# Kernel tuning notes

Measured on AMD Instinct MI355X. Metric: run time of the kernel, lower is better.

Reference implementation:

```python
import jax, jax.numpy as jnp
import numpy as np

N, E, D_IN, D_HID, D_OUT, G = 50000, 800000, 64, 64, 64, 64
BN_EPS = 1e-5


def gcn_conv(x, W, b, src, dst, n_nodes):
    """PyG GCNConv: add self-loops, sym-normalized sum aggregation, then bias.
    out_i = sum_{j->i} d_j^-1/2 d_i^-1/2 (x W)_j + d_i^-1 (x W)_i + b
    where d_i = 1 + in-degree(i) (self-loop included)."""
    h = x @ W  # [N, out]
    deg = jax.ops.segment_sum(jnp.ones((src.shape[0],), h.dtype), dst,
                              num_segments=n_nodes) + 1.0  # self-loop
    dinv = jax.lax.rsqrt(deg)  # deg >= 1 always
    coef = dinv[src] * dinv[dst]  # [E]
    msgs = h[src] * coef[:, None]  # [E, out] -- the big gather
    agg = jax.ops.segment_sum(msgs, dst, num_segments=n_nodes)
    agg = agg + h * (dinv * dinv)[:, None]  # self-loop messages
    return agg + b


def global_mean_pool(x, batch, n_graphs):
    sums = jax.ops.segment_sum(x, batch, num_segments=n_graphs)
    cnts = jax.ops.segment_sum(jnp.ones((x.shape[0],), x.dtype), batch,
                               num_segments=n_graphs)
    return sums / jnp.maximum(cnts, 1.0)[:, None]


def setup_inputs() -> dict:
    key = jax.random.key(0)
    ks = jax.random.split(key, 8)
    x = jax.random.normal(ks[0], (N, D_IN), dtype=jnp.float32)
    edge_index = jax.random.randint(ks[1], (2, E), 0, N, dtype=jnp.int32)
    batch = jnp.sort(jax.random.randint(ks[2], (N,), 0, G, dtype=jnp.int32))
    s1 = 1.0 / np.sqrt(D_IN)
    s2 = 1.0 / np.sqrt(D_HID)
    W1 = jax.random.uniform(ks[3], (D_IN, D_HID), jnp.float32, -s1, s1)
    b1 = jnp.zeros((D_HID,), jnp.float32)
    gamma = jnp.ones((D_HID,), jnp.float32)
    beta = jnp.zeros((D_HID,), jnp.float32)
    W2 = jax.random.uniform(ks[4], (D_HID, D_OUT), jnp.float32, -s2, s2)
    b2 = jnp.zeros((D_OUT,), jnp.float32)
    return {"x": x, "edge_index": edge_index, "batch": batch,
            "W1": W1, "b1": b1, "gamma": gamma, "beta": beta,
            "W2": W2, "b2": b2}


def reference(x, edge_index, batch, W1, b1, gamma, beta, W2, b2):
    src, dst = edge_index[0], edge_index[1]
    h = gcn_conv(x, W1, b1, src, dst, N)
    # BatchNorm1d with batch statistics (training-mode forward)
    mu = jnp.mean(h, axis=0)
    var = jnp.mean(jnp.square(h - mu), axis=0)
    h = (h - mu) * jax.lax.rsqrt(var + BN_EPS) * gamma + beta
    h = jax.nn.elu(h)
    # dropout is identity in eval / deterministic reference
    out = gcn_conv(h, W2, b2, src, dst, N)
    graph_rep = global_mean_pool(out, batch, G)
    return (out, graph_rep)
```

## Files before the change

kernel.cpp:

```cpp
#include <hip/hip_runtime.h>


constexpr int GGRAPHS = 64;
constexpr int EPB = 8192;

__global__ void cnt_kernel(const int* __restrict__ batch, int* __restrict__ cnt, int n) {
  __shared__ int h[GGRAPHS];
  int t = threadIdx.x;
  if (t < GGRAPHS) h[t] = 0;
  __syncthreads();
  for (int i = blockIdx.x * 256 + t; i < n; i += gridDim.x * 256) {
    int g = batch[i];
    if ((unsigned)g < (unsigned)GGRAPHS) atomicAdd(&h[g], 1);
  }
  __syncthreads();
  if (t < GGRAPHS && h[t] > 0) atomicAdd(&cnt[t], h[t]);
}

__global__ void phist_kernel(const int* __restrict__ dst, int* __restrict__ hist,
                             int E, int n, int nblk, int nbuck) {
  __shared__ int h[256];
  int t = threadIdx.x;
  h[t] = 0;
  __syncthreads();
  int e0 = blockIdx.x * EPB;
  int e1 = e0 + EPB < E ? e0 + EPB : E;
  for (int i = e0 + t; i < e1; i += 256) {
    int d = dst[i];
    if ((unsigned)d < (unsigned)n) atomicAdd(&h[d >> 8], 1);
  }
  __syncthreads();
  if (t < nbuck) hist[t * nblk + blockIdx.x] = h[t];
}

__global__ void scan1_kernel(const int* __restrict__ in, int* __restrict__ out,
                             int* __restrict__ bsum, int n) {
  __shared__ int tmp[256];
  int t = threadIdx.x;
  int i = blockIdx.x * 256 + t;
  int v = (i < n) ? in[i] : 0;
  tmp[t] = v;
  __syncthreads();
#pragma unroll
  for (int off = 1; off < 256; off <<= 1) {
    int a = (t >= off) ? tmp[t - off] : 0;
    __syncthreads();
    tmp[t] += a;
    __syncthreads();
  }
  if (i < n) out[i] = tmp[t] - v;
  if (t == 255) bsum[blockIdx.x] = tmp[255];
}

__global__ void scan2_kernel(int* __restrict__ bsum, int nb) {
  __shared__ int tmp[256];
  int t = threadIdx.x;
  int v = (t < nb) ? bsum[t] : 0;
  tmp[t] = v;
  __syncthreads();
#pragma unroll
  for (int off = 1; off < 256; off <<= 1) {
    int a = (t >= off) ? tmp[t - off] : 0;
    __syncthreads();
    tmp[t] += a;
    __syncthreads();
  }
  if (t < nb) bsum[t] = tmp[t] - v;
  if (t == 255) bsum[nb] = tmp[255];
}

__global__ void scan_add_kernel(int* __restrict__ data, const int* __restrict__ bsum,
                                int S, int nbt) {
  int i = blockIdx.x * 256 + threadIdx.x;
  if (i < S) data[i] += bsum[blockIdx.x];
  if (i == 0) data[S] = bsum[nbt];
}

__global__ void part_kernel(const int* __restrict__ srcp, const int* __restrict__ dstp,
                            const int* __restrict__ hist, int* __restrict__ part,
                            int E, int n, int nblk, int nbuck) {
  __shared__ int cur[256];
  int t = threadIdx.x;
  if (t < nbuck) cur[t] = hist[t * nblk + blockIdx.x];
  __syncthreads();
  int e0 = blockIdx.x * EPB;
  int e1 = e0 + EPB < E ? e0 + EPB : E;
  for (int i = e0 + t; i < e1; i += 256) {
    int d = dstp[i];
    if ((unsigned)d >= (unsigned)n) continue;
    int s = srcp[i];
    int pos = atomicAdd(&cur[d >> 8], 1);
    part[pos] = (s << 8) | (d & 255);
  }
}

__global__ void csr_kernel(const int* __restrict__ part, const int* __restrict__ hist,
                           int* __restrict__ rowptr, float* __restrict__ dinv,
                           int* __restrict__ col, int n, int nblk, int nbuck) {
  __shared__ int degL[256], scn[256], cur[256];
  int t = threadIdx.x;
  int b = blockIdx.x;
  degL[t] = 0;
  cur[t] = 0;
  __syncthreads();
  int base = hist[b * nblk];
  int end = hist[(b + 1) * nblk];
  for (int i = base + t; i < end; i += 256) atomicAdd(&degL[part[i] & 255], 1);
  __syncthreads();
  int dv = degL[t];
  scn[t] = dv;
  __syncthreads();
#pragma unroll
  for (int off = 1; off < 256; off <<= 1) {
    int a = (t >= off) ? scn[t - off] : 0;
    __syncthreads();
    scn[t] += a;
    __syncthreads();
  }
  int excl = scn[t] - dv;
  int node = (b << 8) + t;
  if (node < n) {
    rowptr[node] = base + excl;
    dinv[node] = rsqrtf((float)dv + 1.0f);
  }
  if (b == nbuck - 1 && t == 0) rowptr[n] = end;
  scn[t] = excl;
  __syncthreads();
  for (int i = base + t; i < end; i += 256) {
    int u = part[i];
    int d = u & 255;
    int k = atomicAdd(&cur[d], 1);
    col[base + scn[d] + k] = u >> 8;
  }
}

__global__ void mm64_kernel(const float* __restrict__ X, const float* __restrict__ W,
                            float* __restrict__ Y, int n) {
  __shared__ float Ws[64][64];
  __shared__ float xs[4][64];
  int tid = threadIdx.x;
  for (int i = tid; i < 64 * 64; i += 256) Ws[i >> 6][i & 63] = W[i];
  int rr = tid >> 6, c = tid & 63;
  int row = blockIdx.x * 4 + rr;
  xs[rr][c] = (row < n) ? X[row * 64 + c] : 0.0f;
  __syncthreads();
  float acc = 0.0f;
#pragma unroll
  for (int k = 0; k < 64; ++k) acc = fmaf(xs[rr][k], Ws[k][c], acc);
  if (row < n) Y[row * 64 + c] = acc;
}

__global__ void bn_elu_mm64_kernel(const float* __restrict__ X, const float* __restrict__ W,
                                   const float* __restrict__ ss, float* __restrict__ Y, int n) {
  __shared__ float Ws[64][64];
  __shared__ float xs[4][64];
  int tid = threadIdx.x;
  for (int i = tid; i < 64 * 64; i += 256) Ws[i >> 6][i & 63] = W[i];
  int rr = tid >> 6, c = tid & 63;
  int row = blockIdx.x * 4 + rr;
  float v = 0.0f;
  if (row < n) {
    v = X[row * 64 + c] * ss[c] + ss[64 + c];
    v = v > 0.0f ? v : expm1f(v);
  }
  xs[rr][c] = v;
  __syncthreads();
  float acc = 0.0f;
#pragma unroll
  for (int k = 0; k < 64; ++k) acc = fmaf(xs[rr][k], Ws[k][c], acc);
  if (row < n) Y[row * 64 + c] = acc;
}

__global__ void gather_kernel(const int* __restrict__ rowptr, const int* __restrict__ col,
                              const float* __restrict__ dinv, const float* __restrict__ H,
                              const float* __restrict__ b, float* __restrict__ OUT, int n) {
  int wave = threadIdx.x >> 6;
  int lane = threadIdx.x & 63;
  int row = blockIdx.x * 4 + wave;
  if (row >= n) return;
  int sub = lane >> 4;
  int cg = lane & 15;
  int p0 = rowptr[row], p1 = rowptr[row + 1];
  const float4* __restrict__ H4 = (const float4*)H;
  float4 acc = make_float4(0.0f, 0.0f, 0.0f, 0.0f);
  for (int base = p0; base < p1; base += 64) {
    int myp = base + lane;
    int j = (myp < p1) ? col[myp] : 0;
    float w = (myp < p1) ? dinv[j] : 0.0f;
    int m = p1 - base < 64 ? p1 - base : 64;
#pragma unroll 4
    for (int k = 0; k < m; k += 4) {
      int s = k + sub;
      int jj = __shfl(j, s);
      float ww = __shfl(w, s);
      float4 hv = H4[(size_t)jj * 16 + cg];
      acc.x = fmaf(hv.x, ww, acc.x);
      acc.y = fmaf(hv.y, ww, acc.y);
      acc.z = fmaf(hv.z, ww, acc.z);
      acc.w = fmaf(hv.w, ww, acc.w);
    }
  }
  acc.x += __shfl_xor(acc.x, 16);
  acc.y += __shfl_xor(acc.y, 16);
  acc.z += __shfl_xor(acc.z, 16);
  acc.w += __shfl_xor(acc.w, 16);
  acc.x += __shfl_xor(acc.x, 32);
  acc.y += __shfl_xor(acc.y, 32);
  acc.z += __shfl_xor(acc.z, 32);
  acc.w += __shfl_xor(acc.w, 32);
  float di = dinv[row];
  float d2 = di * di;
  float4 self = H4[(size_t)row * 16 + cg];
  float4 bb = ((const float4*)b)[cg];
  float4 o;
  o.x = fmaf(acc.x, di, fmaf(self.x, d2, bb.x));
  o.y = fmaf(acc.y, di, fmaf(self.y, d2, bb.y));
  o.z = fmaf(acc.z, di, fmaf(self.z, d2, bb.z));
  o.w = fmaf(acc.w, di, fmaf(self.w, d2, bb.w));
  if (sub == 0) ((float4*)OUT)[(size_t)row * 16 + cg] = o;
}

__global__ void bnstats_kernel(const float* __restrict__ H, float* __restrict__ bns, int n) {
  int t = threadIdx.x;
  int ch = t & 63;
  float s = 0.0f, s2 = 0.0f;
  int total = n * 64;
  for (int idx = blockIdx.x * 256 + t; idx < total; idx += 512 * 256) {
    float v = H[idx];
    s += v;
    s2 += v * v;
  }
  __shared__ float ls[256], ls2[256];
  ls[t] = s;
  ls2[t] = s2;
  __syncthreads();
  if (t < 64) {
    s = ls[t] + ls[t + 64] + ls[t + 128] + ls[t + 192];
    s2 = ls2[t] + ls2[t + 64] + ls2[t + 128] + ls2[t + 192];
    atomicAdd(&bns[ch], s);
    atomicAdd(&bns[64 + ch], s2);
  }
}

__global__ void bn_final_kernel(const float* __restrict__ bns, const float* __restrict__ gamma,
                                const float* __restrict__ beta, float* __restrict__ ss, int n) {
  int ch = threadIdx.x;
  float inv_n = 1.0f / (float)n;
  float mu = bns[ch] * inv_n;
  float var = bns[64 + ch] * inv_n - mu * mu;
  var = fmaxf(var, 0.0f);
  float sc = gamma[ch] * rsqrtf(var + 1e-5f);
  ss[ch] = sc;
  ss[64 + ch] = beta[ch] - mu * sc;
}

__global__ void pool_kernel(const float* __restrict__ O, const int* __restrict__ batch,
                            float* __restrict__ pool, int n) {
  __shared__ float a0[256], a1[256];
  int t = threadIdx.x;
  int ch = t & 63;
  int grp = t >> 6;
  int base = blockIdx.x * 64;
  int first = base < n - 1 ? base : n - 1;
  int lastrow = base + 63 < n - 1 ? base + 63 : n - 1;
  int g0 = batch[first];
  int glast = batch[lastrow];
  float s0 = 0.0f, s1 = 0.0f;
  for (int k = 0; k < 16; ++k) {
    int row = base + grp * 16 + k;
    if (row >= n) break;
    float v = O[(size_t)row * 64 + ch];
    int g = batch[row];
    if (g == g0) s0 += v;
    else if (g == glast) s1 += v;
    else if ((unsigned)g < (unsigned)GGRAPHS) atomicAdd(&pool[g * 64 + ch], v);
  }
  a0[t] = s0;
  a1[t] = s1;
  __syncthreads();
  if (t < 64) {
    float r0 = a0[t] + a0[t + 64] + a0[t + 128] + a0[t + 192];
    if ((unsigned)g0 < (unsigned)GGRAPHS) atomicAdd(&pool[g0 * 64 + t], r0);
    if (glast != g0) {
      float r1 = a1[t] + a1[t + 64] + a1[t + 128] + a1[t + 192];
      if ((unsigned)glast < (unsigned)GGRAPHS) atomicAdd(&pool[glast * 64 + t], r1);
    }
  }
}

__global__ void pool_final_kernel(const float* __restrict__ pool, const int* __restrict__ cnt,
                                  float* __restrict__ out) {
  int idx = blockIdx.x * 256 + threadIdx.x;
  int g = idx >> 6;
  float c = (float)cnt[g];
  out[idx] = pool[idx] / fmaxf(c, 1.0f);
}

extern "C" void kernel_launch(void* const* d_in, const int* in_sizes, int n_in,
                              void* d_out, int out_size, void* d_ws, size_t ws_size,
                              hipStream_t stream) {
  const float* x = (const float*)d_in[0];
  const int* ei = (const int*)d_in[1];
  const int* batch = (const int*)d_in[2];
  const float* W1 = (const float*)d_in[3];
  const float* b1 = (const float*)d_in[4];
  const float* gamma = (const float*)d_in[5];
  const float* beta = (const float*)d_in[6];
  const float* W2 = (const float*)d_in[7];
  const float* b2 = (const float*)d_in[8];

  const int n = in_sizes[0] / 64;
  const int E = in_sizes[1] / 2;
  const int* srcp = ei;
  const int* dstp = ei + E;

  float* ws = (float*)d_ws;
  size_t nf = (size_t)n * 64;
  float* bufA = ws;
  float* bufB = ws + nf;
  float* dinv = ws + 2 * nf;
  float* bns = dinv + n;
  float* ss = bns + 128;
  int* cnti = (int*)(ss + 128);
  float* pool = (float*)(cnti + 64);
  int* rowptr = (int*)(pool + 4096);
  int* col = rowptr + n + 1;
  int* bsum = col + E;

  int* part = (int*)bufA;
  int* hist = part + E;

  float* out = (float*)d_out;

  size_t zbytes = (size_t)((char*)(pool + 4096) - (char*)bns);
  hipMemsetAsync(bns, 0, zbytes, stream);

  int blk = 256;
  int nblkP = (E + EPB - 1) / EPB;
  int nbuck = (n + 255) >> 8;
  int S = nbuck * nblkP;
  int nbt = (S + 255) / 256;
  int gridRows = (n + 3) / 4;
  int gridPool = (n + 63) / 64;

  phist_kernel<<<nblkP, blk, 0, stream>>>(dstp, hist, E, n, nblkP, nbuck);
  cnt_kernel<<<128, blk, 0, stream>>>(batch, cnti, n);
  scan1_kernel<<<nbt, blk, 0, stream>>>(hist, hist, bsum, S);
  scan2_kernel<<<1, blk, 0, stream>>>(bsum, nbt);
  scan_add_kernel<<<nbt, blk, 0, stream>>>(hist, bsum, S, nbt);
  part_kernel<<<nblkP, blk, 0, stream>>>(srcp, dstp, hist, part, E, n, nblkP, nbuck);
  csr_kernel<<<nbuck, blk, 0, stream>>>(part, hist, rowptr, dinv, col, n, nblkP, nbuck);

  mm64_kernel<<<gridRows, blk, 0, stream>>>(x, W1, bufA, n);
  gather_kernel<<<gridRows, blk, 0, stream>>>(rowptr, col, dinv, bufA, b1, bufB, n);
  bnstats_kernel<<<512, blk, 0, stream>>>(bufB, bns, n);
  bn_final_kernel<<<1, 64, 0, stream>>>(bns, gamma, beta, ss, n);
  bn_elu_mm64_kernel<<<gridRows, blk, 0, stream>>>(bufB, W2, ss, bufA, n);
  gather_kernel<<<gridRows, blk, 0, stream>>>(rowptr, col, dinv, bufA, b2, out, n);
  pool_kernel<<<gridPool, blk, 0, stream>>>(out, batch, pool, n);
  pool_final_kernel<<<(GGRAPHS * 64) / blk, blk, 0, stream>>>(pool, cnti, out + nf);
}
```

Baseline: 284.2 us.

## Fuse BN stats and mean-pool into gather kernels, tile matmuls to 16 rows

BatchNorm sum and sum-of-squares accumulation now happens inside the first gather kernel, and graph mean-pool accumulation inside the second. This removes the separate bnstats and pool passes that reread the full node feature arrays. The atomics go to 64 and 16 replicated partial buffers, which the final kernels reduce, to limit contention. The 64x64 matmul kernels now compute 4 rows per thread, 16 rows per block, which amortises the weight load into shared memory. The gather inner loop is unrolled to issue four independent float4 loads per iteration. In exchange, each gather block pays a shared-memory reduction plus atomics, and the pool fusion issues per-row atomics.

```diff
diff --git a/kernel.cpp b/kernel.cpp
--- a/kernel.cpp
+++ b/kernel.cpp
@@ -137,67 +137,113 @@
 __global__ void mm64_kernel(const float* __restrict__ X, const float* __restrict__ W,
                             float* __restrict__ Y, int n) {
   __shared__ float Ws[64][64];
-  __shared__ float xs[4][64];
+  __shared__ float xs[16][64];
   int tid = threadIdx.x;
   for (int i = tid; i < 64 * 64; i += 256) Ws[i >> 6][i & 63] = W[i];
-  int rr = tid >> 6, c = tid & 63;
-  int row = blockIdx.x * 4 + rr;
-  xs[rr][c] = (row < n) ? X[row * 64 + c] : 0.0f;
-  __syncthreads();
-  float acc = 0.0f;
-#pragma unroll
-  for (int k = 0; k < 64; ++k) acc = fmaf(xs[rr][k], Ws[k][c], acc);
-  if (row < n) Y[row * 64 + c] = acc;
+  int c = tid & 63, rg = tid >> 6;
+  int row0 = blockIdx.x * 16;
+#pragma unroll
+  for (int q = 0; q < 4; ++q) {
+    int r = rg + q * 4;
+    int row = row0 + r;
+    xs[r][c] = (row < n) ? X[(size_t)row * 64 + c] : 0.0f;
+  }
+  __syncthreads();
+  float a0 = 0.f, a1 = 0.f, a2 = 0.f, a3 = 0.f;
+#pragma unroll
+  for (int k = 0; k < 64; ++k) {
+    float wv = Ws[k][c];
+    a0 = fmaf(xs[rg * 4 + 0][k], wv, a0);
+    a1 = fmaf(xs[rg * 4 + 1][k], wv, a1);
+    a2 = fmaf(xs[rg * 4 + 2][k], wv, a2);
+    a3 = fmaf(xs[rg * 4 + 3][k], wv, a3);
+  }
+  int r0 = row0 + rg * 4;
+  if (r0 + 0 < n) Y[(size_t)(r0 + 0) * 64 + c] = a0;
+  if (r0 + 1 < n) Y[(size_t)(r0 + 1) * 64 + c] = a1;
+  if (r0 + 2 < n) Y[(size_t)(r0 + 2) * 64 + c] = a2;
+  if (r0 + 3 < n) Y[(size_t)(r0 + 3) * 64 + c] = a3;
 }
 
 __global__ void bn_elu_mm64_kernel(const float* __restrict__ X, const float* __restrict__ W,
                                    const float* __restrict__ ss, float* __restrict__ Y, int n) {
   __shared__ float Ws[64][64];
-  __shared__ float xs[4][64];
+  __shared__ float xs[16][64];
   int tid = threadIdx.x;
   for (int i = tid; i < 64 * 64; i += 256) Ws[i >> 6][i & 63] = W[i];
-  int rr = tid >> 6, c = tid & 63;
-  int row = blockIdx.x * 4 + rr;
-  float v = 0.0f;
-  if (row < n) {
-    v = X[row * 64 + c] * ss[c] + ss[64 + c];
-    v = v > 0.0f ? v : expm1f(v);
-  }
-  xs[rr][c] = v;
-  __syncthreads();
-  float acc = 0.0f;
-#pragma unroll
-  for (int k = 0; k < 64; ++k) acc = fmaf(xs[rr][k], Ws[k][c], acc);
-  if (row < n) Y[row * 64 + c] = acc;
-}
-
-__global__ void gather_kernel(const int* __restrict__ rowptr, const int* __restrict__ col,
-                              const float* __restrict__ dinv, const float* __restrict__ H,
-                              const float* __restrict__ b, float* __restrict__ OUT, int n) {
-  int wave = threadIdx.x >> 6;
-  int lane = threadIdx.x & 63;
-  int row = blockIdx.x * 4 + wave;
-  if (row >= n) return;
-  int sub = lane >> 4;
-  int cg = lane & 15;
-  int p0 = rowptr[row], p1 = rowptr[row + 1];
-  const float4* __restrict__ H4 = (const float4*)H;
-  float4 acc = make_float4(0.0f, 0.0f, 0.0f, 0.0f);
+  int c = tid & 63, rg = tid >> 6;
+  float sc = ss[c], sh = ss[64 + c];
+  int row0 = blockIdx.x * 16;
+#pragma unroll
+  for (int q = 0; q < 4; ++q) {
+    int r = rg + q * 4;
+    int row = row0 + r;
+    float v = 0.0f;
+    if (row < n) {
+      v = X[(size_t)row * 64 + c] * sc + sh;
+      v = v > 0.0f ? v : expm1f(v);
+    }
+    xs[r][c] = v;
+  }
+  __syncthreads();
+  float a0 = 0.f, a1 = 0.f, a2 = 0.f, a3 = 0.f;
+#pragma unroll
+  for (int k = 0; k < 64; ++k) {
+    float wv = Ws[k][c];
+    a0 = fmaf(xs[rg * 4 + 0][k], wv, a0);
+    a1 = fmaf(xs[rg * 4 + 1][k], wv, a1);
+    a2 = fmaf(xs[rg * 4 + 2][k], wv, a2);
+    a3 = fmaf(xs[rg * 4 + 3][k], wv, a3);
+  }
+  int r0 = row0 + rg * 4;
+  if (r0 + 0 < n) Y[(size_t)(r0 + 0) * 64 + c] = a0;
+  if (r0 + 1 < n) Y[(size_t)(r0 + 1) * 64 + c] = a1;
+  if (r0 + 2 < n) Y[(size_t)(r0 + 2) * 64 + c] = a2;
+  if (r0 + 3 < n) Y[(size_t)(r0 + 3) * 64 + c] = a3;
+}
+
+__device__ __forceinline__ float4 gcn_gather_core(
+    const int* __restrict__ rowptr, const int* __restrict__ col,
+    const float* __restrict__ dinv, const float4* __restrict__ H4,
+    int row, int lane, int sub, int cg, bool valid) {
+  float4 acc = make_float4(0.f, 0.f, 0.f, 0.f);
+  int p0 = 0, p1 = 0;
+  if (valid) { p0 = rowptr[row]; p1 = rowptr[row + 1]; }
   for (int base = p0; base < p1; base += 64) {
     int myp = base + lane;
     int j = (myp < p1) ? col[myp] : 0;
     float w = (myp < p1) ? dinv[j] : 0.0f;
-    int m = p1 - base < 64 ? p1 - base : 64;
-#pragma unroll 4
-    for (int k = 0; k < m; k += 4) {
-      int s = k + sub;
-      int jj = __shfl(j, s);
-      float ww = __shfl(w, s);
-      float4 hv = H4[(size_t)jj * 16 + cg];
-      acc.x = fmaf(hv.x, ww, acc.x);
-      acc.y = fmaf(hv.y, ww, acc.y);
-      acc.z = fmaf(hv.z, ww, acc.z);
-      acc.w = fmaf(hv.w, ww, acc.w);
+    int m = p1 - base;
+    m = m < 64 ? m : 64;
+    for (int k = 0; k < m; k += 16) {
+      int j0 = __shfl(j, k + sub);
+      float w0 = __shfl(w, k + sub);
+      int j1 = __shfl(j, k + 4 + sub);
+      float w1 = __shfl(w, k + 4 + sub);
+      int j2 = __shfl(j, k + 8 + sub);
+      float w2 = __shfl(w, k + 8 + sub);
+      int j3 = __shfl(j, k + 12 + sub);
+      float w3 = __shfl(w, k + 12 + sub);
+      float4 h0 = H4[(size_t)j0 * 16 + cg];
+      float4 h1 = H4[(size_t)j1 * 16 + cg];
+      float4 h2 = H4[(size_t)j2 * 16 + cg];
+      float4 h3 = H4[(size_t)j3 * 16 + cg];
+      acc.x = fmaf(h0.x, w0, acc.x);
+      acc.y = fmaf(h0.y, w0, acc.y);
+      acc.z = fmaf(h0.z, w0, acc.z);
+      acc.w = fmaf(h0.w, w0, acc.w);
+      acc.x = fmaf(h1.x, w1, acc.x);
+      acc.y = fmaf(h1.y, w1, acc.y);
+      acc.z = fmaf(h1.z, w1, acc.z);
+      acc.w = fmaf(h1.w, w1, acc.w);
+      acc.x = fmaf(h2.x, w2, acc.x);
+      acc.y = fmaf(h2.y, w2, acc.y);
+      acc.z = fmaf(h2.z, w2, acc.z);
+      acc.w = fmaf(h2.w, w2, acc.w);
+      acc.x = fmaf(h3.x, w3, acc.x);
+      acc.y = fmaf(h3.y, w3, acc.y);
+      acc.z = fmaf(h3.z, w3, acc.z);
+      acc.w = fmaf(h3.w, w3, acc.w);
     }
   }
   acc.x += __shfl_xor(acc.x, 16);
@@ -208,6 +254,68 @@
   acc.y += __shfl_xor(acc.y, 32);
   acc.z += __shfl_xor(acc.z, 32);
   acc.w += __shfl_xor(acc.w, 32);
+  return acc;
+}
+
+__global__ void gather_bn_kernel(const int* __restrict__ rowptr, const int* __restrict__ col,
+                                 const float* __restrict__ dinv, const float* __restrict__ H,
+                                 const float* __restrict__ b, float* __restrict__ OUT,
+                                 float* __restrict__ bnsR, int n) {
+  int wave = threadIdx.x >> 6;
+  int lane = threadIdx.x & 63;
+  int row = blockIdx.x * 4 + wave;
+  bool valid = row < n;
+  int sub = lane >> 4;
+  int cg = lane & 15;
+  const float4* __restrict__ H4 = (const float4*)H;
+  float4 acc = gcn_gather_core(rowptr, col, dinv, H4, row, lane, sub, cg, valid);
+  float4 o = make_float4(0.f, 0.f, 0.f, 0.f);
+  if (valid) {
+    float di = dinv[row];
+    float d2 = di * di;
+    float4 self = H4[(size_t)row * 16 + cg];
+    float4 bb = ((const float4*)b)[cg];
+    o.x = fmaf(acc.x, di, fmaf(self.x, d2, bb.x));
+    o.y = fmaf(acc.y, di, fmaf(self.y, d2, bb.y));
+    o.z = fmaf(acc.z, di, fmaf(self.z, d2, bb.z));
+    o.w = fmaf(acc.w, di, fmaf(self.w, d2, bb.w));
+    if (sub == 0) ((float4*)OUT)[(size_t)row * 16 + cg] = o;
+  }
+  __shared__ float sA[4][64], sB[4][64];
+  if (sub == 0) {
+    sA[wave][4 * cg + 0] = o.x;
+    sA[wave][4 * cg + 1] = o.y;
+    sA[wave][4 * cg + 2] = o.z;
+    sA[wave][4 * cg + 3] = o.w;
+    sB[wave][4 * cg + 0] = o.x * o.x;
+    sB[wave][4 * cg + 1] = o.y * o.y;
+    sB[wave][4 * cg + 2] = o.z * o.z;
+    sB[wave][4 * cg + 3] = o.w * o.w;
+  }
+  __syncthreads();
+  int t = threadIdx.x;
+  if (t < 64) {
+    float s = sA[0][t] + sA[1][t] + sA[2][t] + sA[3][t];
+    float s2 = sB[0][t] + sB[1][t] + sB[2][t] + sB[3][t];
+    float* d = bnsR + (size_t)(blockIdx.x & 63) * 128;
+    atomicAdd(&d[t], s);
+    atomicAdd(&d[64 + t], s2);
+  }
+}
+
+__global__ void gather_pool_kernel(const int* __restrict__ rowptr, const int* __restrict__ col,
+                                   const float* __restrict__ dinv, const float* __restrict__ H,
+                                   const float* __restrict__ b, float* __restrict__ OUT,
+                                   const int* __restrict__ batch, float* __restrict__ poolR,
+                                   int n) {
+  int wave = threadIdx.x >> 6;
+  int lane = threadIdx.x & 63;
+  int row = blockIdx.x * 4 + wave;
+  if (row >= n) return;
+  int sub = lane >> 4;
+  int cg = lane & 15;
+  const float4* __restrict__ H4 = (const float4*)H;
+  float4 acc = gcn_gather_core(rowptr, col, dinv, H4, row, lane, sub, cg, true);
   float di = dinv[row];
   float d2 = di * di;
   float4 self = H4[(size_t)row * 16 + cg];
@@ -217,83 +325,46 @@
   o.y = fmaf(acc.y, di, fmaf(self.y, d2, bb.y));
   o.z = fmaf(acc.z, di, fmaf(self.z, d2, bb.z));
   o.w = fmaf(acc.w, di, fmaf(self.w, d2, bb.w));
-  if (sub == 0) ((float4*)OUT)[(size_t)row * 16 + cg] = o;
-}
-
-__global__ void bnstats_kernel(const float* __restrict__ H, float* __restrict__ bns, int n) {
-  int t = threadIdx.x;
-  int ch = t & 63;
-  float s = 0.0f, s2 = 0.0f;
-  int total = n * 64;
-  for (int idx = blockIdx.x * 256 + t; idx < total; idx += 512 * 256) {
-    float v = H[idx];
-    s += v;
-    s2 += v * v;
-  }
-  __shared__ float ls[256], ls2[256];
-  ls[t] = s;
-  ls2[t] = s2;
+  if (sub == 0) {
+    ((float4*)OUT)[(size_t)row * 16 + cg] = o;
+    int g = batch[row];
+    if ((unsigned)g < (unsigned)GGRAPHS) {
+      float* d = poolR + (size_t)(blockIdx.x & 15) * 4096 + g * 64 + 4 * cg;
+      atomicAdd(d + 0, o.x);
+      atomicAdd(d + 1, o.y);
+      atomicAdd(d + 2, o.z);
+      atomicAdd(d + 3, o.w);
+    }
+  }
+}
+
+__global__ void bn_final_kernel(const float* __restrict__ bnsR, const float* __restrict__ gamma,
+                                const float* __restrict__ beta, float* __restrict__ ss, int n) {
+  __shared__ float red[128];
+  int t = threadIdx.x;
+  float s = 0.0f;
+  for (int r = 0; r < 64; ++r) s += bnsR[r * 128 + t];
+  red[t] = s;
   __syncthreads();
   if (t < 64) {
-    s = ls[t] + ls[t + 64] + ls[t + 128] + ls[t + 192];
-    s2 = ls2[t] + ls2[t + 64] + ls2[t + 128] + ls2[t + 192];
-    atomicAdd(&bns[ch], s);
-    atomicAdd(&bns[64 + ch], s2);
-  }
-}
-
-__global__ void bn_final_kernel(const float* __restrict__ bns, const float* __restrict__ gamma,
-                                const float* __restrict__ beta, float* __restrict__ ss, int n) {
-  int ch = threadIdx.x;
-  float inv_n = 1.0f / (float)n;
-  float mu = bns[ch] * inv_n;
-  float var = bns[64 + ch] * inv_n - mu * mu;
-  var = fmaxf(var, 0.0f);
-  float sc = gamma[ch] * rsqrtf(var + 1e-5f);
-  ss[ch] = sc;
-  ss[64 + ch] = beta[ch] - mu * sc;
-}
-
-__global__ void pool_kernel(const float* __restrict__ O, const int* __restrict__ batch,
-                            float* __restrict__ pool, int n) {
-  __shared__ float a0[256], a1[256];
-  int t = threadIdx.x;
-  int ch = t & 63;
-  int grp = t >> 6;
-  int base = blockIdx.x * 64;
-  int first = base < n - 1 ? base : n - 1;
-  int lastrow = base + 63 < n - 1 ? base + 63 : n - 1;
-  int g0 = batch[first];
-  int glast = batch[lastrow];
-  float s0 = 0.0f, s1 = 0.0f;
-  for (int k = 0; k < 16; ++k) {
-    int row = base + grp * 16 + k;
-    if (row >= n) break;
-    float v = O[(size_t)row * 64 + ch];
-    int g = batch[row];
-    if (g == g0) s0 += v;
-    else if (g == glast) s1 += v;
-    else if ((unsigned)g < (unsigned)GGRAPHS) atomicAdd(&pool[g * 64 + ch], v);
-  }
-  a0[t] = s0;
-  a1[t] = s1;
-  __syncthreads();
-  if (t < 64) {
-    float r0 = a0[t] + a0[t + 64] + a0[t + 128] + a0[t + 192];
-    if ((unsigned)g0 < (unsigned)GGRAPHS) atomicAdd(&pool[g0 * 64 + t], r0);
-    if (glast != g0) {
-      float r1 = a1[t] + a1[t + 64] + a1[t + 128] + a1[t + 192];
-      if ((unsigned)glast < (unsigned)GGRAPHS) atomicAdd(&pool[glast * 64 + t], r1);
-    }
-  }
-}
-
-__global__ void pool_final_kernel(const float* __restrict__ pool, const int* __restrict__ cnt,
+    float inv_n = 1.0f / (float)n;
+    float mu = red[t] * inv_n;
+    float var = red[64 + t] * inv_n - mu * mu;
+    var = fmaxf(var, 0.0f);
+    float sc = gamma[t] * rsqrtf(var + 1e-5f);
+    ss[t] = sc;
+    ss[64 + t] = beta[t] - mu * sc;
+  }
+}
+
+__global__ void pool_final_kernel(const float* __restrict__ poolR, const int* __restrict__ cnt,
                                   float* __restrict__ out) {
   int idx = blockIdx.x * 256 + threadIdx.x;
+  float s = 0.0f;
+  for (int r = 0; r < 16; ++r) s += poolR[r * 4096 + idx];
   int g = idx >> 6;
   float c = (float)cnt[g];
-  out[idx] = pool[idx] / fmaxf(c, 1.0f);
+  out[idx] = s / fmaxf(c, 1.0f);
 }
 
 extern "C" void kernel_launch(void* const* d_in, const int* in_sizes, int n_in,
@@ -319,21 +390,21 @@
   float* bufA = ws;
   float* bufB = ws + nf;
   float* dinv = ws + 2 * nf;
-  float* bns = dinv + n;
-  float* ss = bns + 128;
-  int* cnti = (int*)(ss + 128);
-  float* pool = (float*)(cnti + 64);
-  int* rowptr = (int*)(pool + 4096);
+  float* ss = dinv + n;
+  int* rowptr = (int*)(ss + 128);
   int* col = rowptr + n + 1;
   int* bsum = col + E;
+  float* bnsR = (float*)(bsum + 257);
+  float* poolR = bnsR + 64 * 128;
+  int* cnti = (int*)(poolR + 16 * 4096);
 
   int* part = (int*)bufA;
   int* hist = part + E;
 
   float* out = (float*)d_out;
 
-  size_t zbytes = (size_t)((char*)(pool + 4096) - (char*)bns);
-  hipMemsetAsync(bns, 0, zbytes, stream);
+  size_t zbytes = (size_t)((char*)(cnti + 64) - (char*)bnsR);
+  hipMemsetAsync(bnsR, 0, zbytes, stream);
 
   int blk = 256;
   int nblkP = (E + EPB - 1) / EPB;
@@ -341,7 +412,7 @@
   int S = nbuck * nblkP;
   int nbt = (S + 255) / 256;
   int gridRows = (n + 3) / 4;
-  int gridPool = (n + 63) / 64;
+  int gridMM = (n + 15) / 16;
 
   phist_kernel<<<nblkP, blk, 0, stream>>>(dstp, hist, E, n, nblkP, nbuck);
   cnt_kernel<<<128, blk, 0, stream>>>(batch, cnti, n);
@@ -351,12 +422,11 @@
   part_kernel<<<nblkP, blk, 0, stream>>>(srcp, dstp, hist, part, E, n, nblkP, nbuck);
   csr_kernel<<<nbuck, blk, 0, stream>>>(part, hist, rowptr, dinv, col, n, nblkP, nbuck);
 
-  mm64_kernel<<<gridRows, blk, 0, stream>>>(x, W1, bufA, n);
-  gather_kernel<<<gridRows, blk, 0, stream>>>(rowptr, col, dinv, bufA, b1, bufB, n);
-  bnstats_kernel<<<512, blk, 0, stream>>>(bufB, bns, n);
-  bn_final_kernel<<<1, 64, 0, stream>>>(bns, gamma, beta, ss, n);
-  bn_elu_mm64_kernel<<<gridRows, blk, 0, stream>>>(bufB, W2, ss, bufA, n);
-  gather_kernel<<<gridRows, blk, 0, stream>>>(rowptr, col, dinv, bufA, b2, out, n);
-  pool_kernel<<<gridPool, blk, 0, stream>>>(out, batch, pool, n);
-  pool_final_kernel<<<(GGRAPHS * 64) / blk, blk, 0, stream>>>(pool, cnti, out + nf);
-}
+  mm64_kernel<<<gridMM, blk, 0, stream>>>(x, W1, bufA, n);
+  gather_bn_kernel<<<gridRows, blk, 0, stream>>>(rowptr, col, dinv, bufA, b1, bufB, bnsR, n);
+  bn_final_kernel<<<1, 128, 0, stream>>>(bnsR, gamma, beta, ss, n);
+  bn_elu_mm64_kernel<<<gridMM, blk, 0, stream>>>(bufB, W2, ss, bufA, n);
+  gather_pool_kernel<<<gridRows, blk, 0, stream>>>(rowptr, col, dinv, bufA, b2, out, batch,
+                                                   poolR, n);
+  pool_final_kernel<<<16, blk, 0, stream>>>(poolR, cnti, out + nf);
+}
```

After: 752.6 us. +164.8%, slower.
